# Kernel optimization log

Hardware: AMD Instinct MI355X
Metric: run time of the kernel (lower is better)

The kernel has to match this reference:

```python
import jax, jax.numpy as jnp
import numpy as np

B, C, H, W = 32, 64, 64, 64
NUM_CODES = 1024
COMMITMENT_COST = 0.25


def setup_inputs() -> dict:
    key = jax.random.key(0)
    k1, k2 = jax.random.split(key)
    z = jax.random.normal(k1, (B, C, H, W), dtype=jnp.float32)
    # matches nn.Embedding init uniform_(-1/num_codes, 1/num_codes)
    codebook = jax.random.uniform(k2, (NUM_CODES, C), dtype=jnp.float32,
                                  minval=-1.0 / NUM_CODES, maxval=1.0 / NUM_CODES)
    return {"z": z, "codebook": codebook}


def reference(z, codebook):
    # b c h w -> b h w c
    zt = jnp.transpose(z, (0, 2, 3, 1))
    b, h, w, c = zt.shape
    z_flat = zt.reshape(-1, c)  # (N, c)

    # squared L2 distances to each code: ||z||^2 + ||e||^2 - 2 z.e
    d = (jnp.sum(z_flat * z_flat, axis=1, keepdims=True)
         + jnp.sum(codebook * codebook, axis=1)[None, :]
         - 2.0 * z_flat @ codebook.T)  # (N, K)
    indices = jnp.argmin(d, axis=1)  # (N,)

    z_q = codebook[indices].reshape(b, h, w, c)

    codebook_loss = jnp.mean((z_q - jax.lax.stop_gradient(zt)) ** 2)
    commitment_loss = jnp.mean((zt - jax.lax.stop_gradient(z_q)) ** 2)
    loss = codebook_loss + COMMITMENT_COST * commitment_loss

    # straight-through estimator
    z_q_st = zt + jax.lax.stop_gradient(z_q - zt)
    z_q_out = jnp.transpose(z_q_st, (0, 3, 1, 2))  # b h w c -> b c h w
    return z_q_out, loss, indices.reshape(b, h, w)
```

## Files before the change

### kernel.cpp

```cpp
#include <hip/hip_runtime.h>

#define CDIM 64
#define KCODES 1024
#define ZQ_ELEMS (32 * 64 * 64 * 64)
#define NROWS 131072
#define FLT_BIG 3.402823466e38f
#define RPB 128
#define NBLK (NROWS / RPB)
#define CSTRIDE 49
#define DELTA 5e-4f

#define WS_BSQ_OFF 16384
#define WS_E1_OFF  32768

#define SK_RD_OFF 25088
#define SK_RK_OFF (25088 + 1024)
#define E_OFF     27136
#define B_OFF     (27136 + 8192)
#define SU_BYTES  (27136 + 8192 + 4096)

typedef __bf16 bf16x8 __attribute__((ext_vector_type(8)));
typedef float  f32x4  __attribute__((ext_vector_type(4)));

__device__ __forceinline__ float pairwise_sq64(const float* v) {
    float r[8];
    #pragma unroll
    for (int j = 0; j < 8; ++j) r[j] = __fmul_rn(v[j], v[j]);
    #pragma unroll
    for (int m = 1; m < 8; ++m) {
        #pragma unroll
        for (int j = 0; j < 8; ++j)
            r[j] = __fadd_rn(r[j], __fmul_rn(v[8 * m + j], v[8 * m + j]));
    }
    return __fadd_rn(__fadd_rn(__fadd_rn(r[0], r[1]), __fadd_rn(r[2], r[3])),
                     __fadd_rn(__fadd_rn(r[4], r[5]), __fadd_rn(r[6], r[7])));
}

__global__ __launch_bounds__(256) void vq_prep(const float* __restrict__ cb,
                                               float* __restrict__ Bsq,
                                               __bf16* __restrict__ e1) {
    const int k = blockIdx.x * 256 + threadIdx.x;
    const float* __restrict__ ck = cb + k * CDIM;
    float v[CDIM];
    #pragma unroll
    for (int q = 0; q < 16; ++q) {
        float4 t = ((const float4*)ck)[q];
        v[4 * q + 0] = t.x; v[4 * q + 1] = t.y; v[4 * q + 2] = t.z; v[4 * q + 3] = t.w;
    }
    Bsq[k] = pairwise_sq64(v);

    const int t = k >> 4, kin = k & 15;
    bf16x8* F1 = (bf16x8*)e1;
    #pragma unroll
    for (int ks = 0; ks < 2; ++ks) {
        #pragma unroll
        for (int g = 0; g < 4; ++g) {
            bf16x8 a;
            #pragma unroll
            for (int i = 0; i < 8; ++i) a[i] = (__bf16)v[ks * 32 + 8 * g + i];
            F1[(t * 2 + ks) * 64 + ((g << 4) | kin)] = a;
        }
    }
}

#define INS(s, j, accv, Bv, code0) \
    { \
        const float vv = __fmaf_rn(-2.f, (accv), (Bv)); \
        const float kk = __int_as_float((__float_as_int(vv) & 0xFFFFFC00) | (code0)); \
        const float o0 = K0[s][j], o1 = K1[s][j], o2 = K2[s][j]; \
        K0[s][j] = fminf(o0, kk); \
        K1[s][j] = __builtin_amdgcn_fmed3f(o0, o1, kk); \
        K2[s][j] = __builtin_amdgcn_fmed3f(o1, o2, kk); \
    }

#define TILE_COMPUTE(Ea, Eb, code0) \
    { \
        const float Bv = sB[code0]; \
        f32x4 a0 = __builtin_amdgcn_mfma_f32_16x16x32_bf16(zh00, Ea, zero, 0, 0, 0); \
        a0       = __builtin_amdgcn_mfma_f32_16x16x32_bf16(zh01, Eb, a0, 0, 0, 0); \
        f32x4 a1 = __builtin_amdgcn_mfma_f32_16x16x32_bf16(zh10, Ea, zero, 0, 0, 0); \
        a1       = __builtin_amdgcn_mfma_f32_16x16x32_bf16(zh11, Eb, a1, 0, 0, 0); \
        INS(0, 0, a0[0], Bv, code0) INS(0, 1, a0[1], Bv, code0) \
        INS(0, 2, a0[2], Bv, code0) INS(0, 3, a0[3], Bv, code0) \
        INS(1, 0, a1[0], Bv, code0) INS(1, 1, a1[1], Bv, code0) \
        INS(1, 2, a1[2], Bv, code0) INS(1, 3, a1[3], Bv, code0) \
    }

__global__ __launch_bounds__(256, 4) void vq_main(const float* __restrict__ z,
                                                  const float* __restrict__ cb,
                                                  const float* __restrict__ Bsq,
                                                  const __bf16* __restrict__ e1,
                                                  float* __restrict__ zq_out,
                                                  float* __restrict__ idx_out,
                                                  double* __restrict__ part) {
    __shared__ __align__(16) unsigned char sU[SU_BYTES];
    __shared__ double sP2[2];
    float* __restrict__ sB = (float*)(sU + B_OFF);

    const int tid = threadIdx.x;
    const int n0 = blockIdx.x * RPB;
    const int b = n0 >> 12;
    const int hw0 = n0 & 4095;
    const float* __restrict__ zb = z + ((size_t)b << 18) + hw0;

    for (int k = tid; k < KCODES; k += 256) sB[k] = Bsq[k];

    {
        bf16x8* __restrict__ zfw = (bf16x8*)sU;
        const int r = tid & 127;
        const int h = tid >> 7;
        const int w = r >> 5, s = (r >> 4) & 1, li = r & 15;
        #pragma unroll
        for (int g = 0; g < 4; ++g) {
            bf16x8 hi;
            #pragma unroll
            for (int i = 0; i < 8; ++i) {
                const float fv = zb[((size_t)(32 * h + 8 * g + i) << 12) + r];
                hi[i] = (__bf16)fv;
            }
            zfw[(w * 4 + s * 2 + h) * 65 + ((g << 4) | li)] = hi;
        }
        *(float4*)(sU + E_OFF + tid * 16) =
            *(const float4*)((const unsigned char*)e1 + tid * 16);
    }
    __syncthreads();

    const int lane = tid & 63, w = tid >> 6;
    const int g = lane >> 4, li = lane & 15;

    const bf16x8* __restrict__ zf = (const bf16x8*)sU;
    const bf16x8 zh00 = zf[(w * 4 + 0) * 65 + lane];
    const bf16x8 zh01 = zf[(w * 4 + 1) * 65 + lane];
    const bf16x8 zh10 = zf[(w * 4 + 2) * 65 + lane];
    const bf16x8 zh11 = zf[(w * 4 + 3) * 65 + lane];

    float K0[2][4], K1[2][4], K2[2][4];
    #pragma unroll
    for (int s = 0; s < 2; ++s)
        #pragma unroll
        for (int j = 0; j < 4; ++j) { K0[s][j] = FLT_BIG; K1[s][j] = FLT_BIG; K2[s][j] = FLT_BIG; }

    const f32x4 zero = {0.f, 0.f, 0.f, 0.f};

    float4 vP = *(const float4*)((const unsigned char*)e1 + 4096 + tid * 16);

    for (int c = 0; c < 32; ++c) {
        const float4 vN =
            *(const float4*)((const unsigned char*)e1 + (c + 2) * 4096 + tid * 16);
        *(float4*)(sU + E_OFF + ((c + 1) & 1) * 4096 + tid * 16) = vP;

        const bf16x8* __restrict__ buf = (const bf16x8*)(sU + E_OFF + (c & 1) * 4096);
        const int cb0 = c * 32 + li;
        TILE_COMPUTE(buf[lane],       buf[64 + lane],  cb0)
        TILE_COMPUTE(buf[128 + lane], buf[192 + lane], cb0 + 16)

        vP = vN;
        asm volatile("s_waitcnt lgkmcnt(0)" ::: "memory");
        __builtin_amdgcn_s_barrier();
        __builtin_amdgcn_sched_barrier(0);
    }

    __syncthreads();

    float* __restrict__ sKey = (float*)sU;
    float* __restrict__ sRd = (float*)(sU + SK_RD_OFF);
    int*   __restrict__ sRk = (int*)(sU + SK_RK_OFF);
    #pragma unroll
    for (int s = 0; s < 2; ++s) {
        #pragma unroll
        for (int j = 0; j < 4; ++j) {
            const int row = 32 * w + 16 * s + 4 * g + j;
            const int base = row * CSTRIDE + li * 3;
            sKey[base + 0] = K0[s][j];
            sKey[base + 1] = K1[s][j];
            sKey[base + 2] = K2[s][j];
        }
    }
    __syncthreads();

    {
        const int r = tid & 127;
        const int half = tid >> 7;
        const int n = n0 + r;

        float gmin = FLT_BIG;
        #pragma unroll
        for (int s2 = 0; s2 < 48; ++s2) gmin = fminf(gmin, sKey[r * CSTRIDE + s2]);
        const float thr = gmin + DELTA;

        float zrow[CDIM];
        const float* __restrict__ zp = zb + r;
        #pragma unroll
        for (int c = 0; c < CDIM; ++c) zrow[c] = zp[(size_t)c << 12];
        const float A = pairwise_sq64(zrow);

        float bd = FLT_BIG;
        int bk = 1 << 30;
        const int sbeg = half * 24;
        for (int s2 = sbeg; s2 < sbeg + 24; ++s2) {
            const float kv = sKey[r * CSTRIDE + s2];
            if (kv <= thr) {
                const int k = __float_as_int(kv) & 0x3FF;
                const float4* __restrict__ ek = (const float4*)(cb + (size_t)k * CDIM);
                float m = 0.f;
                #pragma unroll
                for (int q = 0; q < 16; ++q) {
                    float4 e = ek[q];
                    m = __fmaf_rn(zrow[4 * q + 0], e.x, m);
                    m = __fmaf_rn(zrow[4 * q + 1], e.y, m);
                    m = __fmaf_rn(zrow[4 * q + 2], e.z, m);
                    m = __fmaf_rn(zrow[4 * q + 3], e.w, m);
                }
                const float d = __fsub_rn(__fadd_rn(A, sB[k]), __fadd_rn(m, m));
                if (d < bd || (d == bd && k < bk)) { bd = d; bk = k; }
            }
        }

        if (half == 1) { sRd[r] = bd; sRk[r] = bk; }
        __syncthreads();

        if (tid < RPB) {
            const float d1 = sRd[r];
            const int   k1 = sRk[r];
            if (d1 < bd || (d1 == bd && k1 < bk)) { bd = d1; bk = k1; }

            idx_out[n] = (float)bk;

            const float4* __restrict__ cq = (const float4*)(cb + (size_t)bk * CDIM);
            float* __restrict__ zo = zq_out + ((size_t)b << 18) + hw0 + r;
            float lsum = 0.f;
            #pragma unroll
            for (int q = 0; q < 16; ++q) {
                float4 qv = cq[q];
                zo[(size_t)(4 * q + 0) << 12] = qv.x;
                zo[(size_t)(4 * q + 1) << 12] = qv.y;
                zo[(size_t)(4 * q + 2) << 12] = qv.z;
                zo[(size_t)(4 * q + 3) << 12] = qv.w;
                lsum = fmaf(qv.x - zrow[4 * q + 0], qv.x - zrow[4 * q + 0], lsum);
                lsum = fmaf(qv.y - zrow[4 * q + 1], qv.y - zrow[4 * q + 1], lsum);
                lsum = fmaf(qv.z - zrow[4 * q + 2], qv.z - zrow[4 * q + 2], lsum);
                lsum = fmaf(qv.w - zrow[4 * q + 3], qv.w - zrow[4 * q + 3], lsum);
            }

            double ls = (double)lsum;
            for (int off = 32; off > 0; off >>= 1) ls += __shfl_down(ls, off, 64);
            if ((tid & 63) == 0) sP2[tid >> 6] = ls;
        }
    }
    __syncthreads();
    if (tid == 0) part[blockIdx.x] = sP2[0] + sP2[1];
}

__global__ void vq_finalize(const double* __restrict__ part, float* __restrict__ loss_out) {
    __shared__ double s[16];
    const int tid = threadIdx.x;
    double v = part[tid];
    for (int off = 32; off > 0; off >>= 1) v += __shfl_down(v, off, 64);
    if ((tid & 63) == 0) s[tid >> 6] = v;
    __syncthreads();
    if (tid == 0) {
        double t = 0.0;
        #pragma unroll
        for (int i = 0; i < 16; ++i) t += s[i];
        *loss_out = (float)(1.25 * t / (double)ZQ_ELEMS);
    }
}

extern "C" void kernel_launch(void* const* d_in, const int* in_sizes, int n_in,
                              void* d_out, int out_size, void* d_ws, size_t ws_size,
                              hipStream_t stream) {
    const float* z  = (const float*)d_in[0];
    const float* cb = (const float*)d_in[1];
    float* out  = (float*)d_out;
    float* zq   = out;
    float* loss = out + ZQ_ELEMS;
    float* idx  = out + ZQ_ELEMS + 1;
    char* ws = (char*)d_ws;
    double* part = (double*)ws;
    float* Bsq   = (float*)(ws + WS_BSQ_OFF);
    __bf16* e1   = (__bf16*)(ws + WS_E1_OFF);

    vq_prep<<<4, 256, 0, stream>>>(cb, Bsq, e1);
    vq_main<<<NBLK, 256, 0, stream>>>(z, cb, Bsq, e1, zq, idx, part);
    vq_finalize<<<1, 1024, 0, stream>>>(part, loss);
}
```

Baseline: 69.88 us.

## Split fused VQ kernel into MFMA screening and exact rescue kernels

```diff
diff --git a/kernel.cpp b/kernel.cpp
--- a/kernel.cpp
+++ b/kernel.cpp
@@ -7,17 +7,15 @@
 #define FLT_BIG 3.402823466e38f
 #define RPB 128
 #define NBLK (NROWS / RPB)
-#define CSTRIDE 49
 #define DELTA 5e-4f
 
 #define WS_BSQ_OFF 16384
 #define WS_E1_OFF  32768
-
-#define SK_RD_OFF 25088
-#define SK_RK_OFF (25088 + 1024)
-#define E_OFF     27136
-#define B_OFF     (27136 + 8192)
-#define SU_BYTES  (27136 + 8192 + 4096)
+#define WS_KEY_OFF 262144
+
+#define E_OFF     16640
+#define B_OFF     24832
+#define SU_BYTES  28928
 
 typedef __bf16 bf16x8 __attribute__((ext_vector_type(8)));
 typedef float  f32x4  __attribute__((ext_vector_type(4)));
@@ -86,15 +84,11 @@
         INS(1, 2, a1[2], Bv, code0) INS(1, 3, a1[3], Bv, code0) \
     }
 
-__global__ __launch_bounds__(256, 4) void vq_main(const float* __restrict__ z,
-                                                  const float* __restrict__ cb,
-                                                  const float* __restrict__ Bsq,
-                                                  const __bf16* __restrict__ e1,
-                                                  float* __restrict__ zq_out,
-                                                  float* __restrict__ idx_out,
-                                                  double* __restrict__ part) {
+__global__ __launch_bounds__(256, 4) void vq_screen(const float* __restrict__ z,
+                                                    const float* __restrict__ Bsq,
+                                                    const __bf16* __restrict__ e1,
+                                                    float* __restrict__ keys) {
     __shared__ __align__(16) unsigned char sU[SU_BYTES];
-    __shared__ double sP2[2];
     float* __restrict__ sB = (float*)(sU + B_OFF);
 
     const int tid = threadIdx.x;
@@ -160,99 +154,96 @@
         __builtin_amdgcn_sched_barrier(0);
     }
 
-    __syncthreads();
-
-    float* __restrict__ sKey = (float*)sU;
-    float* __restrict__ sRd = (float*)(sU + SK_RD_OFF);
-    int*   __restrict__ sRk = (int*)(sU + SK_RK_OFF);
     #pragma unroll
     for (int s = 0; s < 2; ++s) {
         #pragma unroll
         for (int j = 0; j < 4; ++j) {
             const int row = 32 * w + 16 * s + 4 * g + j;
-            const int base = row * CSTRIDE + li * 3;
-            sKey[base + 0] = K0[s][j];
-            sKey[base + 1] = K1[s][j];
-            sKey[base + 2] = K2[s][j];
-        }
-    }
-    __syncthreads();
-
-    {
-        const int r = tid & 127;
-        const int half = tid >> 7;
-        const int n = n0 + r;
-
-        float gmin = FLT_BIG;
-        #pragma unroll
-        for (int s2 = 0; s2 < 48; ++s2) gmin = fminf(gmin, sKey[r * CSTRIDE + s2]);
-        const float thr = gmin + DELTA;
-
-        float zrow[CDIM];
-        const float* __restrict__ zp = zb + r;
-        #pragma unroll
-        for (int c = 0; c < CDIM; ++c) zrow[c] = zp[(size_t)c << 12];
-        const float A = pairwise_sq64(zrow);
-
-        float bd = FLT_BIG;
-        int bk = 1 << 30;
-        const int sbeg = half * 24;
-        for (int s2 = sbeg; s2 < sbeg + 24; ++s2) {
-            const float kv = sKey[r * CSTRIDE + s2];
-            if (kv <= thr) {
-                const int k = __float_as_int(kv) & 0x3FF;
-                const float4* __restrict__ ek = (const float4*)(cb + (size_t)k * CDIM);
-                float m = 0.f;
-                #pragma unroll
-                for (int q = 0; q < 16; ++q) {
-                    float4 e = ek[q];
-                    m = __fmaf_rn(zrow[4 * q + 0], e.x, m);
-                    m = __fmaf_rn(zrow[4 * q + 1], e.y, m);
-                    m = __fmaf_rn(zrow[4 * q + 2], e.z, m);
-                    m = __fmaf_rn(zrow[4 * q + 3], e.w, m);
-                }
-                const float d = __fsub_rn(__fadd_rn(A, sB[k]), __fadd_rn(m, m));
-                if (d < bd || (d == bd && k < bk)) { bd = d; bk = k; }
-            }
-        }
-
-        if (half == 1) { sRd[r] = bd; sRk[r] = bk; }
-        __syncthreads();
-
-        if (tid < RPB) {
-            const float d1 = sRd[r];
-            const int   k1 = sRk[r];
-            if (d1 < bd || (d1 == bd && k1 < bk)) { bd = d1; bk = k1; }
-
-            idx_out[n] = (float)bk;
-
-            const float4* __restrict__ cq = (const float4*)(cb + (size_t)bk * CDIM);
-            float* __restrict__ zo = zq_out + ((size_t)b << 18) + hw0 + r;
-            float lsum = 0.f;
+            float* __restrict__ gk = keys + (size_t)(n0 + row) * 48 + li * 3;
+            gk[0] = K0[s][j];
+            gk[1] = K1[s][j];
+            gk[2] = K2[s][j];
+        }
+    }
+}
+
+__global__ __launch_bounds__(256) void vq_rescue(const float* __restrict__ z,
+                                                 const float* __restrict__ cb,
+                                                 const float* __restrict__ Bsq,
+                                                 const float* __restrict__ keys,
+                                                 float* __restrict__ zq_out,
+                                                 float* __restrict__ idx_out,
+                                                 double* __restrict__ part) {
+    __shared__ double sW[4];
+    const int tid = threadIdx.x;
+    const int n = blockIdx.x * 256 + tid;
+    const int b = n >> 12;
+    const int hw = n & 4095;
+
+    const float* __restrict__ krow = keys + (size_t)n * 48;
+
+    float gmin = FLT_BIG;
+    #pragma unroll
+    for (int q = 0; q < 12; ++q) {
+        float4 kv4 = ((const float4*)krow)[q];
+        gmin = fminf(gmin, fminf(fminf(kv4.x, kv4.y), fminf(kv4.z, kv4.w)));
+    }
+    const float thr = gmin + DELTA;
+
+    float zrow[CDIM];
+    const float* __restrict__ zp = z + ((size_t)b << 18) + hw;
+    #pragma unroll
+    for (int c = 0; c < CDIM; ++c) zrow[c] = zp[(size_t)c << 12];
+    const float A = pairwise_sq64(zrow);
+
+    float bd = FLT_BIG;
+    int bk = 1 << 30;
+    for (int s2 = 0; s2 < 48; ++s2) {
+        const float kv = krow[s2];
+        if (kv <= thr) {
+            const int k = __float_as_int(kv) & 0x3FF;
+            const float4* __restrict__ ek = (const float4*)(cb + (size_t)k * CDIM);
+            float m = 0.f;
             #pragma unroll
             for (int q = 0; q < 16; ++q) {
-                float4 qv = cq[q];
-                zo[(size_t)(4 * q + 0) << 12] = qv.x;
-                zo[(size_t)(4 * q + 1) << 12] = qv.y;
-                zo[(size_t)(4 * q + 2) << 12] = qv.z;
-                zo[(size_t)(4 * q + 3) << 12] = qv.w;
-                lsum = fmaf(qv.x - zrow[4 * q + 0], qv.x - zrow[4 * q + 0], lsum);
-                lsum = fmaf(qv.y - zrow[4 * q + 1], qv.y - zrow[4 * q + 1], lsum);
-                lsum = fmaf(qv.z - zrow[4 * q + 2], qv.z - zrow[4 * q + 2], lsum);
-                lsum = fmaf(qv.w - zrow[4 * q + 3], qv.w - zrow[4 * q + 3], lsum);
+                float4 e = ek[q];
+                m = __fmaf_rn(zrow[4 * q + 0], e.x, m);
+                m = __fmaf_rn(zrow[4 * q + 1], e.y, m);
+                m = __fmaf_rn(zrow[4 * q + 2], e.z, m);
+                m = __fmaf_rn(zrow[4 * q + 3], e.w, m);
             }
-
-            double ls = (double)lsum;
-            for (int off = 32; off > 0; off >>= 1) ls += __shfl_down(ls, off, 64);
-            if ((tid & 63) == 0) sP2[tid >> 6] = ls;
-        }
-    }
+            const float d = __fsub_rn(__fadd_rn(A, Bsq[k]), __fadd_rn(m, m));
+            if (d < bd || (d == bd && k < bk)) { bd = d; bk = k; }
+        }
+    }
+
+    idx_out[n] = (float)bk;
+
+    const float4* __restrict__ cq = (const float4*)(cb + (size_t)bk * CDIM);
+    float* __restrict__ zo = zq_out + ((size_t)b << 18) + hw;
+    float lsum = 0.f;
+    #pragma unroll
+    for (int q = 0; q < 16; ++q) {
+        float4 qv = cq[q];
+        zo[(size_t)(4 * q + 0) << 12] = qv.x;
+        zo[(size_t)(4 * q + 1) << 12] = qv.y;
+        zo[(size_t)(4 * q + 2) << 12] = qv.z;
+        zo[(size_t)(4 * q + 3) << 12] = qv.w;
+        lsum = fmaf(qv.x - zrow[4 * q + 0], qv.x - zrow[4 * q + 0], lsum);
+        lsum = fmaf(qv.y - zrow[4 * q + 1], qv.y - zrow[4 * q + 1], lsum);
+        lsum = fmaf(qv.z - zrow[4 * q + 2], qv.z - zrow[4 * q + 2], lsum);
+        lsum = fmaf(qv.w - zrow[4 * q + 3], qv.w - zrow[4 * q + 3], lsum);
+    }
+
+    double ls = (double)lsum;
+    for (int off = 32; off > 0; off >>= 1) ls += __shfl_down(ls, off, 64);
+    if ((tid & 63) == 0) sW[tid >> 6] = ls;
     __syncthreads();
-    if (tid == 0) part[blockIdx.x] = sP2[0] + sP2[1];
+    if (tid == 0) part[blockIdx.x] = sW[0] + sW[1] + sW[2] + sW[3];
 }
 
 __global__ void vq_finalize(const double* __restrict__ part, float* __restrict__ loss_out) {
-    __shared__ double s[16];
+    __shared__ double s[8];
     const int tid = threadIdx.x;
     double v = part[tid];
     for (int off = 32; off > 0; off >>= 1) v += __shfl_down(v, off, 64);
@@ -261,7 +252,7 @@
     if (tid == 0) {
         double t = 0.0;
         #pragma unroll
-        for (int i = 0; i < 16; ++i) t += s[i];
+        for (int i = 0; i < 8; ++i) t += s[i];
         *loss_out = (float)(1.25 * t / (double)ZQ_ELEMS);
     }
 }
@@ -279,8 +270,10 @@
     double* part = (double*)ws;
     float* Bsq   = (float*)(ws + WS_BSQ_OFF);
     __bf16* e1   = (__bf16*)(ws + WS_E1_OFF);
+    float* keys  = (float*)(ws + WS_KEY_OFF);
 
     vq_prep<<<4, 256, 0, stream>>>(cb, Bsq, e1);
-    vq_main<<<NBLK, 256, 0, stream>>>(z, cb, Bsq, e1, zq, idx, part);
-    vq_finalize<<<1, 1024, 0, stream>>>(part, loss);
-}
+    vq_screen<<<NBLK, 256, 0, stream>>>(z, Bsq, e1, keys);
+    vq_rescue<<<512, 256, 0, stream>>>(z, cb, Bsq, keys, zq, idx, part);
+    vq_finalize<<<1, 512, 0, stream>>>(part, loss);
+}
```

Result: slower. 107.6 us (+53.9%).
